# Kernel tuning notes

Measured on AMD Instinct MI355X. Metric: run time of the kernel, lower is better.

The kernel has to match this reference:

```python
import jax, jax.numpy as jnp
import numpy as np

B, S, H, N, D = 2, 2048, 1024, 16, 64  # batch, seq, hidden, heads, head_size
PAD = -30000.0


def setup_inputs() -> dict:
    key = jax.random.key(0)
    kx, kqkv, kout, krpe = jax.random.split(key, 4)
    x = jax.random.normal(kx, (B, S, H), jnp.float32)
    qkv = jax.random.normal(kqkv, (H, 3, N, D), jnp.float32) * H ** (-0.5)
    out_w = jax.random.normal(kout, (N, D, H), jnp.float32) * (N * D) ** (-0.5)
    # rpe_bias is zero-init in torch; use small randn so the bias path is exercised
    rpe_bias = jax.random.normal(krpe, (N, S), jnp.float32) * 0.02
    return {"x": x, "qkv": qkv, "out_w": out_w, "rpe_bias": rpe_bias}


def reference(x, qkv, out_w, rpe_bias):
    # q, k, v: [B, N, S, D]
    q, k, v = jnp.einsum('bsx,xMnd->Mbnsd', x, qkv)
    s = x.shape[1]
    a = jnp.einsum('bnsd,bntd->bnst', q, k) * q.shape[-1] ** (-0.5)
    # cumulative relative-position bias: bias[n, i, j] = cumsum(rpe)[n, i-j] for i>=j,
    # PAD otherwise (exactly what to_tril produces on the row-broadcast cumsum).
    cum = jnp.cumsum(rpe_bias[:, :s], axis=-1)            # [N, S]
    rel = jnp.arange(s)[:, None] - jnp.arange(s)[None, :]  # [S, S], i - j
    bias = jnp.where(rel >= 0, cum[:, jnp.clip(rel, 0)], PAD)  # [N, S, S]
    a = jax.nn.softmax(a + bias, axis=-1)
    mix = jnp.einsum('bnst,bntd->bnsd', a, v)
    return jnp.einsum('bnsd,ndx->bsx', mix, out_w)
```

## Files before the change

### kernel.cpp

```cpp
#include <hip/hip_runtime.h>
#include <hip/hip_bf16.h>
#include <cstdint>
#include <cstddef>

#define B_   2
#define S_   2048
#define H_   1024
#define NH   16
#define DH   64
#define SCALE 0.125f

typedef __hip_bfloat16 bf16;
typedef short bf16x8 __attribute__((ext_vector_type(8)));
typedef float f32x4 __attribute__((ext_vector_type(4)));

#define MFMA16(a, b, c) __builtin_amdgcn_mfma_f32_16x16x32_bf16((a), (b), (c), 0, 0, 0)

__device__ __forceinline__ void async16(const void* g, void* l) {
  __builtin_amdgcn_global_load_lds(
      (const __attribute__((address_space(1))) void*)g,
      (__attribute__((address_space(3))) void*)l,
      16, 0, 0);
}

__global__ void convert_f32_bf16(const float* __restrict__ src, bf16* __restrict__ dst,
                                 int n) {
  int i = (blockIdx.x * 256 + threadIdx.x) * 4;
  if (i + 3 < n) {
    float4 v = *(const float4*)(src + i);
    dst[i + 0] = __float2bfloat16(v.x);
    dst[i + 1] = __float2bfloat16(v.y);
    dst[i + 2] = __float2bfloat16(v.z);
    dst[i + 3] = __float2bfloat16(v.w);
  }
}

__global__ void transpose_f32_bf16(const float* __restrict__ src, bf16* __restrict__ dst,
                                   int R, int C) {
  __shared__ bf16 tile[32][33];
  int c0 = blockIdx.x * 32, r0 = blockIdx.y * 32;
  int tx = threadIdx.x & 31, ty = threadIdx.x >> 5;
  for (int i = 0; i < 32; i += 8)
    tile[ty + i][tx] = __float2bfloat16(src[(size_t)(r0 + ty + i) * C + c0 + tx]);
  __syncthreads();
  for (int i = 0; i < 32; i += 8)
    dst[(size_t)(c0 + ty + i) * R + r0 + tx] = tile[tx][ty + i];
}

__global__ void rpe_scan(const float* __restrict__ rpe, float* __restrict__ cum) {
  __shared__ float ssum[256];
  int n = blockIdx.x, t = threadIdx.x;
  float loc[8];
  float s = 0.f;
  int base = t * 8;
  for (int u = 0; u < 8; ++u) {
    loc[u] = rpe[n * S_ + base + u];
    s += loc[u];
  }
  ssum[t] = s;
  __syncthreads();
  float own = s;
  for (int off = 1; off < 256; off <<= 1) {
    float v = (t >= off) ? ssum[t - off] : 0.f;
    __syncthreads();
    ssum[t] += v;
    __syncthreads();
  }
  float run = ssum[t] - own;
  for (int u = 0; u < 8; ++u) {
    run += loc[u];
    cum[n * S_ + base + u] = run;
  }
}

template <int MODE>
__global__ __launch_bounds__(256, 2)
void gemm_bt(const bf16* __restrict__ A, const bf16* __restrict__ Bt,
             bf16* __restrict__ C0, bf16* __restrict__ C1, bf16* __restrict__ C2,
             float* __restrict__ F0) {
  __shared__ char smem[MODE == 0 ? 36864 : 16384] __attribute__((aligned(16)));
  bf16* As = (bf16*)smem;
  bf16* Bs = (bf16*)(smem + 8192);
  const int tid = threadIdx.x, lane = tid & 63, w = tid >> 6;
  const int lr = lane & 15, lq = lane >> 4;
  const int m0 = blockIdx.y * 128, n0 = blockIdx.x * 128;
  const int wm = (w & 1) * 64, wn = (w >> 1) * 64;

  f32x4 acc[4][4] = {};

  for (int k0 = 0; k0 < 1024; k0 += 32) {
    __syncthreads();
    for (int t = 0; t < 2; ++t) {
      int c = (t * 4 + w) * 64 + lane;
      int row = c >> 2, ch = c & 3;
      int k8 = (ch ^ ((row >> 1) & 3)) * 8;
      async16(A + (size_t)(m0 + row) * 1024 + k0 + k8,
              (char*)As + (size_t)(t * 4 + w) * 1024 + lane * 16);
      async16(Bt + (size_t)(n0 + row) * 1024 + k0 + k8,
              (char*)Bs + (size_t)(t * 4 + w) * 1024 + lane * 16);
    }
    __syncthreads();
    bf16x8 af[4], bfr[4];
#pragma unroll
    for (int mt = 0; mt < 4; ++mt) {
      int row = wm + mt * 16 + lr;
      af[mt] = *(const bf16x8*)(As + row * 32 + ((lq ^ ((row >> 1) & 3)) << 3));
    }
#pragma unroll
    for (int nt = 0; nt < 4; ++nt) {
      int row = wn + nt * 16 + lr;
      bfr[nt] = *(const bf16x8*)(Bs + row * 32 + ((lq ^ ((row >> 1) & 3)) << 3));
    }
#pragma unroll
    for (int mt = 0; mt < 4; ++mt)
#pragma unroll
      for (int nt = 0; nt < 4; ++nt)
        acc[mt][nt] = MFMA16(af[mt], bfr[nt], acc[mt][nt]);
  }

  if (MODE == 0) {
    __syncthreads();
    bf16* E = (bf16*)smem + w * (64 * 72);
    const int cbase = n0 + wn;
    const int mm = cbase >> 10, nn = (cbase >> 6) & 15;
    const int bb = (m0 + wm) >> 11;
    const int sbase = (m0 + wm) & 2047;
    if (mm < 2) {
#pragma unroll
      for (int mt = 0; mt < 4; ++mt)
#pragma unroll
        for (int nt = 0; nt < 4; ++nt)
#pragma unroll
          for (int r = 0; r < 4; ++r)
            E[(mt * 16 + lq * 4 + r) * 72 + nt * 16 + lr] =
                __float2bfloat16(acc[mt][nt][r]);
      bf16* dst = (mm == 0 ? C0 : C1) +
                  ((size_t)(bb * NH + nn) * S_ + sbase) * DH;
#pragma unroll
      for (int it = 0; it < 8; ++it) {
        int c = it * 64 + lane;
        int rw = c >> 3, c8 = c & 7;
        *(uint4*)(dst + (size_t)rw * DH + c8 * 8) =
            *(const uint4*)(E + rw * 72 + c8 * 8);
      }
    } else {
#pragma unroll
      for (int mt = 0; mt < 4; ++mt)
#pragma unroll
        for (int nt = 0; nt < 4; ++nt)
#pragma unroll
          for (int r = 0; r < 4; ++r)
            E[(nt * 16 + lr) * 72 + mt * 16 + lq * 4 + r] =
                __float2bfloat16(acc[mt][nt][r]);
      bf16* dst = C2 + (size_t)(bb * NH + nn) * DH * S_;
#pragma unroll
      for (int it = 0; it < 8; ++it) {
        int c = it * 64 + lane;
        int dr = c >> 3, c8 = c & 7;
        *(uint4*)(dst + (size_t)dr * S_ + sbase + c8 * 8) =
            *(const uint4*)(E + dr * 72 + c8 * 8);
      }
    }
  } else {
#pragma unroll
    for (int mt = 0; mt < 4; ++mt)
#pragma unroll
      for (int nt = 0; nt < 4; ++nt)
#pragma unroll
        for (int r = 0; r < 4; ++r) {
          int rM = m0 + wm + mt * 16 + lq * 4 + r;
          int cN = n0 + wn + nt * 16 + lr;
          F0[(size_t)rM * 1024 + cN] = acc[mt][nt][r];
        }
  }
}

__global__ __launch_bounds__(256, 3)
void fa_kernel(const bf16* __restrict__ q, const bf16* __restrict__ k,
               const bf16* __restrict__ vt, const float* __restrict__ cum,
               bf16* __restrict__ mix) {
  __shared__ char smem[51200] __attribute__((aligned(16)));
  bf16* Ps = (bf16*)(smem + 32768);
  float* cumbuf = (float*)(smem + 50176);

  const int tid = threadIdx.x, lane = tid & 63, w = tid >> 6;
  const int lr = lane & 15, lq = lane >> 4;

  const int L = blockIdx.x;
  const int xcd = L & 7, slot = L >> 3;
  const int bn = xcd + 8 * (slot >> 5);
  const int ti = 31 - (slot & 31);
  const int n = bn & (NH - 1);
  const int b = bn >> 4;
  const float* cumn = cum + n * S_;

  const int i0 = ti * 64;
  const int nj = (ti >> 1) + 1;

  const bf16* qbase = q + ((size_t)bn * S_ + i0 + w * 16) * DH;
  bf16x8 qf[2];
#pragma unroll
  for (int kt = 0; kt < 2; ++kt)
    qf[kt] = *(const bf16x8*)(qbase + lr * DH + kt * 32 + lq * 8);

  f32x4 oacc[4] = {};
  float m_i = -1e30f, l_i = 0.f;
  const int iloc = w * 16 + lr;

  for (int jt = 0; jt < nj; ++jt) {
    const int j0 = jt * 128;
    const bool diag = (jt == nj - 1);
    __syncthreads();

    const char* ksrc = (const char*)(k + ((size_t)bn * S_ + j0) * DH);
#pragma unroll
    for (int t = 0; t < 4; ++t) {
      int cb = t * 4 + w;
      int row = cb * 8 + (lane >> 3);
      int cs = (lane & 7) ^ (row & 7);
      async16(ksrc + row * 128 + cs * 16, smem + cb * 1024 + lane * 16);
    }
    const char* vsrc = (const char*)(vt + (size_t)bn * DH * S_);
#pragma unroll
    for (int t = 0; t < 4; ++t) {
      int cb = t * 4 + w;
      int row = cb * 4 + (lane >> 4);
      int cs = (lane & 15) ^ (row & 15);
      async16(vsrc + (size_t)row * (S_ * 2) + j0 * 2 + cs * 16,
              smem + 16384 + cb * 1024 + lane * 16);
    }
    {
      int src = i0 - j0 - 127 + tid;
      src = src < 0 ? 0 : (src > S_ - 1 ? S_ - 1 : src);
      cumbuf[tid] = cumn[src];
    }
    __syncthreads();

    f32x4 sa[8] = {};
#pragma unroll
    for (int kt = 0; kt < 2; ++kt)
#pragma unroll
      for (int nt = 0; nt < 8; ++nt) {
        int krow = nt * 16 + lr;
        bf16x8 kf = *(const bf16x8*)(smem + krow * 128 +
                        (((kt * 4 + lq) ^ (krow & 7)) << 4));
        sa[nt] = MFMA16(kf, qf[kt], sa[nt]);
      }

    const int doff = i0 - j0;
    float rmax = -1e30f;
    if (!diag) {
#pragma unroll
      for (int nt = 0; nt < 8; ++nt)
#pragma unroll
        for (int r = 0; r < 4; ++r) {
          int rel = iloc - nt * 16 - lq * 4 - r;
          float val = sa[nt][r] * SCALE + cumbuf[127 + rel];
          sa[nt][r] = val;
          rmax = fmaxf(rmax, val);
        }
    } else {
#pragma unroll
      for (int nt = 0; nt < 8; ++nt)
#pragma unroll
        for (int r = 0; r < 4; ++r) {
          int rel = iloc - nt * 16 - lq * 4 - r;
          float val = (doff + rel >= 0) ? sa[nt][r] * SCALE + cumbuf[127 + rel]
                                        : -1e30f;
          sa[nt][r] = val;
          rmax = fmaxf(rmax, val);
        }
    }
    float mx = fmaxf(rmax, __shfl_xor(rmax, 16));
    mx = fmaxf(mx, __shfl_xor(mx, 32));
    float newm = fmaxf(m_i, mx);
    float al = __expf(m_i - newm);
    m_i = newm;
    float rs = 0.f;
#pragma unroll
    for (int nt = 0; nt < 8; ++nt)
#pragma unroll
      for (int r = 0; r < 4; ++r) {
        float p = __expf(sa[nt][r] - newm);
        sa[nt][r] = p;
        rs += p;
      }
    rs += __shfl_xor(rs, 16);
    rs += __shfl_xor(rs, 32);
    l_i = l_i * al + rs;
    float alr[4];
#pragma unroll
    for (int r = 0; r < 4; ++r) alr[r] = __shfl(al, lq * 4 + r);
#pragma unroll
    for (int dt = 0; dt < 4; ++dt)
#pragma unroll
      for (int r = 0; r < 4; ++r) oacc[dt][r] *= alr[r];

#pragma unroll
    for (int nt = 0; nt < 8; ++nt) {
      bf16 pk[4];
#pragma unroll
      for (int r = 0; r < 4; ++r) pk[r] = __float2bfloat16(sa[nt][r]);
      *(uint64_t*)(Ps + iloc * 136 + nt * 16 + lq * 4) = *(const uint64_t*)pk;
    }

#pragma unroll
    for (int kt2 = 0; kt2 < 4; ++kt2) {
      bf16x8 pf = *(const bf16x8*)(Ps + (w * 16 + lr) * 136 + kt2 * 32 + lq * 8);
#pragma unroll
      for (int dt = 0; dt < 4; ++dt) {
        int vrow = dt * 16 + lr;
        bf16x8 vf = *(const bf16x8*)(smem + 16384 + vrow * 256 +
                        (((kt2 * 4 + lq) ^ (vrow & 15)) << 4));
        oacc[dt] = MFMA16(pf, vf, oacc[dt]);
      }
    }
  }

  float lr4[4];
#pragma unroll
  for (int r = 0; r < 4; ++r) lr4[r] = __shfl(l_i, lq * 4 + r);
#pragma unroll
  for (int dt = 0; dt < 4; ++dt)
#pragma unroll
    for (int r = 0; r < 4; ++r) {
      int i = i0 + w * 16 + lq * 4 + r;
      int d = dt * 16 + lr;
      mix[((size_t)(b * S_ + i) * NH + n) * DH + d] =
          __float2bfloat16(oacc[dt][r] / lr4[r]);
    }
}

extern "C" void kernel_launch(void* const* d_in, const int* in_sizes, int n_in,
                              void* d_out, int out_size, void* d_ws, size_t ws_size,
                              hipStream_t stream) {
  const float* x     = (const float*)d_in[0];
  const float* qkv   = (const float*)d_in[1];
  const float* out_w = (const float*)d_in[2];
  const float* rpe   = (const float*)d_in[3];
  float* out = (float*)d_out;

  char* ws = (char*)d_ws;
  bf16* qkvT  = (bf16*)(ws + 0);
  bf16* outwT = (bf16*)(ws + 6291456);
  bf16* xb    = (bf16*)(ws + 8388608);
  bf16* qb    = (bf16*)(ws + 16777216);
  bf16* kb    = (bf16*)(ws + 25165824);
  bf16* vtb   = (bf16*)(ws + 33554432);
  bf16* mixb  = (bf16*)(ws + 41943040);
  float* cum  = (float*)(ws + 50331648);

  convert_f32_bf16<<<4096, 256, 0, stream>>>(x, xb, 4096 * 1024);
  transpose_f32_bf16<<<dim3(3072 / 32, 1024 / 32), 256, 0, stream>>>(qkv, qkvT, 1024, 3072);
  transpose_f32_bf16<<<dim3(1024 / 32, 1024 / 32), 256, 0, stream>>>(out_w, outwT, 1024, 1024);
  rpe_scan<<<NH, 256, 0, stream>>>(rpe, cum);
  gemm_bt<0><<<dim3(3072 / 128, 4096 / 128), 256, 0, stream>>>(xb, qkvT, qb, kb, vtb, nullptr);
  fa_kernel<<<1024, 256, 0, stream>>>(qb, kb, vtb, cum, mixb);
  gemm_bt<1><<<dim3(1024 / 128, 4096 / 128), 256, 0, stream>>>(mixb, outwT, nullptr, nullptr, nullptr, out);
}
```

Before: 200.2 us.

## Fuse prep kernels, use exp2 softmax, skip masked diagonal tiles, raise GEMM occupancy

New measurement: 238.3 us. 1.19x slower.

```diff
diff --git a/kernel.cpp b/kernel.cpp
--- a/kernel.cpp
+++ b/kernel.cpp
@@ -8,7 +8,8 @@
 #define H_   1024
 #define NH   16
 #define DH   64
-#define SCALE 0.125f
+#define LOG2E 1.4426950408889634f
+#define SCALE2 (0.125f * LOG2E)
 
 typedef __hip_bfloat16 bf16;
 typedef short bf16x8 __attribute__((ext_vector_type(8)));
@@ -23,23 +24,10 @@
       16, 0, 0);
 }
 
-__global__ void convert_f32_bf16(const float* __restrict__ src, bf16* __restrict__ dst,
-                                 int n) {
-  int i = (blockIdx.x * 256 + threadIdx.x) * 4;
-  if (i + 3 < n) {
-    float4 v = *(const float4*)(src + i);
-    dst[i + 0] = __float2bfloat16(v.x);
-    dst[i + 1] = __float2bfloat16(v.y);
-    dst[i + 2] = __float2bfloat16(v.z);
-    dst[i + 3] = __float2bfloat16(v.w);
-  }
-}
-
-__global__ void transpose_f32_bf16(const float* __restrict__ src, bf16* __restrict__ dst,
-                                   int R, int C) {
-  __shared__ bf16 tile[32][33];
-  int c0 = blockIdx.x * 32, r0 = blockIdx.y * 32;
-  int tx = threadIdx.x & 31, ty = threadIdx.x >> 5;
+__device__ __forceinline__ void tr_body(const float* __restrict__ src,
+                                        bf16* __restrict__ dst, int R, int C,
+                                        int c0, int r0, bf16 (*tile)[33], int tid) {
+  int tx = tid & 31, ty = tid >> 5;
   for (int i = 0; i < 32; i += 8)
     tile[ty + i][tx] = __float2bfloat16(src[(size_t)(r0 + ty + i) * C + c0 + tx]);
   __syncthreads();
@@ -47,34 +35,58 @@
     dst[(size_t)(c0 + ty + i) * R + r0 + tx] = tile[tx][ty + i];
 }
 
-__global__ void rpe_scan(const float* __restrict__ rpe, float* __restrict__ cum) {
-  __shared__ float ssum[256];
-  int n = blockIdx.x, t = threadIdx.x;
-  float loc[8];
-  float s = 0.f;
-  int base = t * 8;
-  for (int u = 0; u < 8; ++u) {
-    loc[u] = rpe[n * S_ + base + u];
-    s += loc[u];
+__global__ __launch_bounds__(256)
+void prep(const float* __restrict__ x, bf16* __restrict__ xb,
+          const float* __restrict__ qkv, bf16* __restrict__ qkvT,
+          const float* __restrict__ outw, bf16* __restrict__ outwT,
+          const float* __restrict__ rpe, float* __restrict__ cum) {
+  __shared__ char pm[2176] __attribute__((aligned(16)));
+  const int L = blockIdx.x, tid = threadIdx.x;
+  if (L < 4096) {
+    int i = (L * 256 + tid) * 4;
+    float4 v = *(const float4*)(x + i);
+    bf16 o[4] = {__float2bfloat16(v.x), __float2bfloat16(v.y),
+                 __float2bfloat16(v.z), __float2bfloat16(v.w)};
+    *(uint64_t*)(xb + i) = *(const uint64_t*)o;
+  } else if (L < 7168) {
+    int t = L - 4096;
+    int cx = t % 96, ry = t / 96;
+    tr_body(qkv, qkvT, 1024, 3072, cx * 32, ry * 32, (bf16(*)[33])pm, tid);
+  } else if (L < 8192) {
+    int t = L - 7168;
+    int cx = t & 31, ry = t >> 5;
+    tr_body(outw, outwT, 1024, 1024, cx * 32, ry * 32, (bf16(*)[33])pm, tid);
+  } else {
+    float* ssum = (float*)pm;
+    int n = L - 8192;
+    float loc[8];
+    float s = 0.f;
+    int base = tid * 8;
+#pragma unroll
+    for (int u = 0; u < 8; ++u) {
+      loc[u] = rpe[n * S_ + base + u];
+      s += loc[u];
+    }
+    ssum[tid] = s;
+    __syncthreads();
+    float own = s;
+    for (int off = 1; off < 256; off <<= 1) {
+      float v = (tid >= off) ? ssum[tid - off] : 0.f;
+      __syncthreads();
+      ssum[tid] += v;
+      __syncthreads();
+    }
+    float run = ssum[tid] - own;
+#pragma unroll
+    for (int u = 0; u < 8; ++u) {
+      run += loc[u];
+      cum[n * S_ + base + u] = run * LOG2E;
+    }
   }
-  ssum[t] = s;
-  __syncthreads();
-  float own = s;
-  for (int off = 1; off < 256; off <<= 1) {
-    float v = (t >= off) ? ssum[t - off] : 0.f;
-    __syncthreads();
-    ssum[t] += v;
-    __syncthreads();
-  }
-  float run = ssum[t] - own;
-  for (int u = 0; u < 8; ++u) {
-    run += loc[u];
-    cum[n * S_ + base + u] = run;
-  }
 }
 
 template <int MODE>
-__global__ __launch_bounds__(256, 2)
+__global__ __launch_bounds__(256, MODE == 0 ? 4 : 2)
 void gemm_bt(const bf16* __restrict__ A, const bf16* __restrict__ Bt,
              bf16* __restrict__ C0, bf16* __restrict__ C1, bf16* __restrict__ C2,
              float* __restrict__ F0) {
@@ -210,11 +222,14 @@
   for (int jt = 0; jt < nj; ++jt) {
     const int j0 = jt * 128;
     const bool diag = (jt == nj - 1);
+    const bool diag0 = diag && (i0 == j0);
+    const int ntK = diag0 ? 4 : 8;
+    const int kt2max = diag0 ? 2 : 4;
     __syncthreads();
 
     const char* ksrc = (const char*)(k + ((size_t)bn * S_ + j0) * DH);
-#pragma unroll
-    for (int t = 0; t < 4; ++t) {
+    const int tmaxK = diag0 ? 2 : 4;
+    for (int t = 0; t < tmaxK; ++t) {
       int cb = t * 4 + w;
       int row = cb * 8 + (lane >> 3);
       int cs = (lane & 7) ^ (row & 7);
@@ -241,10 +256,12 @@
     for (int kt = 0; kt < 2; ++kt)
 #pragma unroll
       for (int nt = 0; nt < 8; ++nt) {
-        int krow = nt * 16 + lr;
-        bf16x8 kf = *(const bf16x8*)(smem + krow * 128 +
-                        (((kt * 4 + lq) ^ (krow & 7)) << 4));
-        sa[nt] = MFMA16(kf, qf[kt], sa[nt]);
+        if (nt < ntK) {
+          int krow = nt * 16 + lr;
+          bf16x8 kf = *(const bf16x8*)(smem + krow * 128 +
+                          (((kt * 4 + lq) ^ (krow & 7)) << 4));
+          sa[nt] = MFMA16(kf, qf[kt], sa[nt]);
+        }
       }
 
     const int doff = i0 - j0;
@@ -255,36 +272,40 @@
 #pragma unroll
         for (int r = 0; r < 4; ++r) {
           int rel = iloc - nt * 16 - lq * 4 - r;
-          float val = sa[nt][r] * SCALE + cumbuf[127 + rel];
+          float val = sa[nt][r] * SCALE2 + cumbuf[127 + rel];
           sa[nt][r] = val;
           rmax = fmaxf(rmax, val);
         }
     } else {
 #pragma unroll
-      for (int nt = 0; nt < 8; ++nt)
-#pragma unroll
-        for (int r = 0; r < 4; ++r) {
-          int rel = iloc - nt * 16 - lq * 4 - r;
-          float val = (doff + rel >= 0) ? sa[nt][r] * SCALE + cumbuf[127 + rel]
-                                        : -1e30f;
-          sa[nt][r] = val;
-          rmax = fmaxf(rmax, val);
-        }
+      for (int nt = 0; nt < 8; ++nt) {
+        if (nt < ntK)
+#pragma unroll
+          for (int r = 0; r < 4; ++r) {
+            int rel = iloc - nt * 16 - lq * 4 - r;
+            float val = (doff + rel >= 0) ? sa[nt][r] * SCALE2 + cumbuf[127 + rel]
+                                          : -1e30f;
+            sa[nt][r] = val;
+            rmax = fmaxf(rmax, val);
+          }
+      }
     }
     float mx = fmaxf(rmax, __shfl_xor(rmax, 16));
     mx = fmaxf(mx, __shfl_xor(mx, 32));
     float newm = fmaxf(m_i, mx);
-    float al = __expf(m_i - newm);
+    float al = exp2f(m_i - newm);
     m_i = newm;
     float rs = 0.f;
 #pragma unroll
-    for (int nt = 0; nt < 8; ++nt)
-#pragma unroll
-      for (int r = 0; r < 4; ++r) {
-        float p = __expf(sa[nt][r] - newm);
-        sa[nt][r] = p;
-        rs += p;
-      }
+    for (int nt = 0; nt < 8; ++nt) {
+      if (nt < ntK)
+#pragma unroll
+        for (int r = 0; r < 4; ++r) {
+          float p = exp2f(sa[nt][r] - newm);
+          sa[nt][r] = p;
+          rs += p;
+        }
+    }
     rs += __shfl_xor(rs, 16);
     rs += __shfl_xor(rs, 32);
     l_i = l_i * al + rs;
@@ -298,21 +319,25 @@
 
 #pragma unroll
     for (int nt = 0; nt < 8; ++nt) {
-      bf16 pk[4];
-#pragma unroll
-      for (int r = 0; r < 4; ++r) pk[r] = __float2bfloat16(sa[nt][r]);
-      *(uint64_t*)(Ps + iloc * 136 + nt * 16 + lq * 4) = *(const uint64_t*)pk;
+      if (nt < ntK) {
+        bf16 pk[4];
+#pragma unroll
+        for (int r = 0; r < 4; ++r) pk[r] = __float2bfloat16(sa[nt][r]);
+        *(uint64_t*)(Ps + iloc * 136 + nt * 16 + lq * 4) = *(const uint64_t*)pk;
+      }
     }
 
 #pragma unroll
     for (int kt2 = 0; kt2 < 4; ++kt2) {
-      bf16x8 pf = *(const bf16x8*)(Ps + (w * 16 + lr) * 136 + kt2 * 32 + lq * 8);
-#pragma unroll
-      for (int dt = 0; dt < 4; ++dt) {
-        int vrow = dt * 16 + lr;
-        bf16x8 vf = *(const bf16x8*)(smem + 16384 + vrow * 256 +
-                        (((kt2 * 4 + lq) ^ (vrow & 15)) << 4));
-        oacc[dt] = MFMA16(pf, vf, oacc[dt]);
+      if (kt2 < kt2max) {
+        bf16x8 pf = *(const bf16x8*)(Ps + (w * 16 + lr) * 136 + kt2 * 32 + lq * 8);
+#pragma unroll
+        for (int dt = 0; dt < 4; ++dt) {
+          int vrow = dt * 16 + lr;
+          bf16x8 vf = *(const bf16x8*)(smem + 16384 + vrow * 256 +
+                          (((kt2 * 4 + lq) ^ (vrow & 15)) << 4));
+          oacc[dt] = MFMA16(pf, vf, oacc[dt]);
+        }
       }
     }
   }
@@ -350,10 +375,7 @@
   bf16* mixb  = (bf16*)(ws + 41943040);
   float* cum  = (float*)(ws + 50331648);
 
-  convert_f32_bf16<<<4096, 256, 0, stream>>>(x, xb, 4096 * 1024);
-  transpose_f32_bf16<<<dim3(3072 / 32, 1024 / 32), 256, 0, stream>>>(qkv, qkvT, 1024, 3072);
-  transpose_f32_bf16<<<dim3(1024 / 32, 1024 / 32), 256, 0, stream>>>(out_w, outwT, 1024, 1024);
-  rpe_scan<<<NH, 256, 0, stream>>>(rpe, cum);
+  prep<<<8208, 256, 0, stream>>>(x, xb, qkv, qkvT, out_w, outwT, rpe, cum);
   gemm_bt<0><<<dim3(3072 / 128, 4096 / 128), 256, 0, stream>>>(xb, qkvT, qb, kb, vtb, nullptr);
   fa_kernel<<<1024, 256, 0, stream>>>(qb, kb, vtb, cum, mixb);
   gemm_bt<1><<<dim3(1024 / 128, 4096 / 128), 256, 0, stream>>>(mixb, outwT, nullptr, nullptr, nullptr, out);
```
